# Kernel tuning notes

Hardware: AMD Instinct MI355X
Metric: run time of the kernel (lower is better)

Reference implementation:

```python
import jax, jax.numpy as jnp
from jax import lax
import numpy as np

S, B, I, H, O = 65536, 1, 2, 128, 1


def setup_inputs() -> dict:
    key = jax.random.key(0)
    k1, k2, k3, k4 = jax.random.split(key, 4)
    # xavier_normal-style scales
    s_ih = (2.0 / (4 * H + I)) ** 0.5
    s_hh = (2.0 / (4 * H + H)) ** 0.5
    s_out = (2.0 / (H + O)) ** 0.5
    return {
        "x": jax.random.normal(k1, (S, B, I), jnp.float32),
        "h0": jnp.zeros((1, B, H), jnp.float32),
        "c0": jnp.zeros((1, B, H), jnp.float32),
        "W_ih": jax.random.normal(k2, (4 * H, I), jnp.float32) * s_ih,
        "W_hh": jax.random.normal(k3, (4 * H, H), jnp.float32) * s_hh,
        "b_ih": jnp.zeros((4 * H,), jnp.float32),
        "b_hh": jnp.zeros((4 * H,), jnp.float32),
        "W_out": jax.random.normal(k4, (O, H), jnp.float32) * s_out,
        "b_out": jnp.zeros((O,), jnp.float32),
    }


def reference(x, h0, c0, W_ih, W_hh, b_ih, b_hh, W_out, b_out):
    # Precompute input-to-gate projections for all timesteps: (S, B, 4H)
    xg = jnp.einsum("sbi,gi->sbg", x, W_ih) + b_ih + b_hh

    def step(carry, xg_t):
        h, c = carry  # (B, H) each
        gates = xg_t + h @ W_hh.T  # (B, 4H); PyTorch order i,f,g,o
        i, f, g, o = jnp.split(gates, 4, axis=-1)
        i = jax.nn.sigmoid(i)
        f = jax.nn.sigmoid(f)
        g = jnp.tanh(g)
        o = jax.nn.sigmoid(o)
        c = f * c + i * g
        h = o * jnp.tanh(c)
        return (h, c), h

    (_, _), hs = lax.scan(step, (h0[0], c0[0]), xg)  # hs: (S, B, H)
    out = jnp.tanh(hs.transpose(1, 0, 2))  # (B, S, H), matches permute(1,0,2)
    out = out @ W_out.T + b_out  # (B, S, O)
    return out.reshape(out.shape[0] * out.shape[1], -1)  # (B*S, O)
```

## Files before the change

kernel.cpp:

```cpp
#include <hip/hip_runtime.h>

#define S_LEN 65536
#define HDIM 128

typedef _Float16 half2_t __attribute__((ext_vector_type(2)));
typedef _Float16 half8_t __attribute__((ext_vector_type(8)));
typedef float f32x4 __attribute__((ext_vector_type(4)));

__device__ __forceinline__ float sigm(float x) {
    return 1.0f / (1.0f + __expf(-x));
}
__device__ __forceinline__ float tanh_fast(float x) {
    return 2.0f / (1.0f + __expf(-2.0f * x)) - 1.0f;
}
__device__ __forceinline__ float dot2(half2_t a, half2_t b, float c) {
#if __has_builtin(__builtin_amdgcn_fdot2)
    return __builtin_amdgcn_fdot2(a, b, c, false);
#else
    return fmaf((float)a.x, (float)b.x, fmaf((float)a.y, (float)b.y, c));
#endif
}

#define WG_BARRIER() do {                                         \
    asm volatile("s_waitcnt lgkmcnt(0)" ::: "memory");            \
    __builtin_amdgcn_s_barrier();                                 \
    asm volatile("" ::: "memory");                                \
} while (0)

__global__ __launch_bounds__(256)
__attribute__((amdgpu_waves_per_eu(1, 1)))
void lstm_seq_dot(const float* __restrict__ x,
                  const float* __restrict__ h0,
                  const float* __restrict__ c0,
                  const float* __restrict__ W_ih,
                  const float* __restrict__ W_hh,
                  const float* __restrict__ b_ih,
                  const float* __restrict__ b_hh,
                  _Float16* __restrict__ h_hist)
{
    __shared__ __align__(16) _Float16 h_buf[2][HDIM];

    const int tid  = threadIdx.x;
    const int lane = tid & 63;
    const int w    = tid >> 6;
    const int j    = lane & 31;
    const int half = lane >> 5;
    const int hidx = w * 32 + j;
    const int k0   = half * 64;

#define LOAD_WF(g, c) \
    half8_t wf_##g##_##c; { \
        const float* s_ = W_hh + (size_t)(hidx + 128 * (g)) * HDIM \
                               + k0 + 8 * (c); \
        wf_##g##_##c = (half8_t){ \
            (_Float16)s_[0], (_Float16)s_[1], (_Float16)s_[2], (_Float16)s_[3], \
            (_Float16)s_[4], (_Float16)s_[5], (_Float16)s_[6], (_Float16)s_[7] }; \
        asm volatile("" : "+v"(wf_##g##_##c)); }
    LOAD_WF(0,0) LOAD_WF(0,1) LOAD_WF(0,2) LOAD_WF(0,3)
    LOAD_WF(0,4) LOAD_WF(0,5) LOAD_WF(0,6) LOAD_WF(0,7)
    LOAD_WF(1,0) LOAD_WF(1,1) LOAD_WF(1,2) LOAD_WF(1,3)
    LOAD_WF(1,4) LOAD_WF(1,5) LOAD_WF(1,6) LOAD_WF(1,7)
    LOAD_WF(2,0) LOAD_WF(2,1) LOAD_WF(2,2) LOAD_WF(2,3)
    LOAD_WF(2,4) LOAD_WF(2,5) LOAD_WF(2,6) LOAD_WF(2,7)
    LOAD_WF(3,0) LOAD_WF(3,1) LOAD_WF(3,2) LOAD_WF(3,3)
    LOAD_WF(3,4) LOAD_WF(3,5) LOAD_WF(3,6) LOAD_WF(3,7)
#undef LOAD_WF

    const int r0 = hidx, r1 = hidx + 128, r2 = hidx + 256, r3 = hidx + 384;
    const float wi00 = W_ih[2 * r0], wi01 = W_ih[2 * r0 + 1];
    const float wi10 = W_ih[2 * r1], wi11 = W_ih[2 * r1 + 1];
    const float wi20 = W_ih[2 * r2], wi21 = W_ih[2 * r2 + 1];
    const float wi30 = W_ih[2 * r3], wi31 = W_ih[2 * r3 + 1];
    const float bs0 = b_ih[r0] + b_hh[r0];
    const float bs1 = b_ih[r1] + b_hh[r1];
    const float bs2 = b_ih[r2] + b_hh[r2];
    const float bs3 = b_ih[r3] + b_hh[r3];
    float c = c0[hidx];

    if (tid < HDIM) h_buf[0][tid] = (_Float16)h0[tid];
    __syncthreads();

    const float2* xp = (const float2*)x;
    float2 xcur = xp[0];
    float2 xn1  = xp[1];

    const half8_t* hb0 = ((const half8_t*)h_buf[0]) + 8 * half;
    const half8_t* hb1 = ((const half8_t*)h_buf[1]) + 8 * half;

    _Float16* hh = h_hist + hidx;

#define DOT8(acc, wv, hv) \
    acc = dot2((half2_t){wv[0], wv[1]}, (half2_t){hv[0], hv[1]}, acc); \
    acc = dot2((half2_t){wv[2], wv[3]}, (half2_t){hv[2], hv[3]}, acc); \
    acc = dot2((half2_t){wv[4], wv[5]}, (half2_t){hv[4], hv[5]}, acc); \
    acc = dot2((half2_t){wv[6], wv[7]}, (half2_t){hv[6], hv[7]}, acc);

#define DCHUNK(a0_, a1_, a2_, a3_, c_, hv) \
    DOT8(a0_, wf_0_##c_, hv) \
    DOT8(a1_, wf_1_##c_, hv) \
    DOT8(a2_, wf_2_##c_, hv) \
    DOT8(a3_, wf_3_##c_, hv)

#define STEP(T, RB, WB, OFF) { \
     \
    half8_t hv0 = (RB)[0], hv1 = (RB)[1], hv2 = (RB)[2], hv3 = (RB)[3]; \
    half8_t hv4 = (RB)[4], hv5 = (RB)[5], hv6 = (RB)[6], hv7 = (RB)[7]; \
    int tn_ = (T) + 2; if (tn_ >= S_LEN) tn_ = S_LEN - 1; \
    float2 xnew_ = xp[tn_]; \
     \
    const float xg0 = fmaf(wi00, xcur.x, fmaf(wi01, xcur.y, bs0)); \
    const float xg1 = fmaf(wi10, xcur.x, fmaf(wi11, xcur.y, bs1)); \
    const float xg2 = fmaf(wi20, xcur.x, fmaf(wi21, xcur.y, bs2)); \
    const float xg3 = fmaf(wi30, xcur.x, fmaf(wi31, xcur.y, bs3)); \
    float sA0 = 0.f, sA1 = 0.f, sA2 = 0.f, sA3 = 0.f; \
    float sB0 = 0.f, sB1 = 0.f, sB2 = 0.f, sB3 = 0.f; \
    DCHUNK(sA0, sA1, sA2, sA3, 0, hv0) \
    DCHUNK(sB0, sB1, sB2, sB3, 1, hv1) \
    DCHUNK(sA0, sA1, sA2, sA3, 2, hv2) \
    DCHUNK(sB0, sB1, sB2, sB3, 3, hv3) \
    DCHUNK(sA0, sA1, sA2, sA3, 4, hv4) \
    DCHUNK(sB0, sB1, sB2, sB3, 5, hv5) \
    DCHUNK(sA0, sA1, sA2, sA3, 6, hv6) \
    DCHUNK(sB0, sB1, sB2, sB3, 7, hv7) \
    float s0 = sA0 + sB0; \
    float s1 = sA1 + sB1; \
    float s2 = sA2 + sB2; \
    float s3 = sA3 + sB3; \
     \
    s0 += __shfl_xor(s0, 32, 64); \
    s1 += __shfl_xor(s1, 32, 64); \
    s2 += __shfl_xor(s2, 32, 64); \
    s3 += __shfl_xor(s3, 32, 64); \
    const float gi = sigm(s0 + xg0); \
    const float gf = sigm(s1 + xg1); \
    const float gg = tanh_fast(s2 + xg2); \
    const float go = sigm(s3 + xg3); \
    c = fmaf(gf, c, gi * gg); \
    const float hvx_ = go * tanh_fast(c); \
    const _Float16 hf_ = (_Float16)hvx_; \
    if (lane < 32) { \
        (WB)[hidx] = hf_;                  \
        hh[OFF] = hf_;                     \
    } \
    xcur = xn1; xn1 = xnew_; \
    WG_BARRIER(); }

    #pragma unroll 1
    for (int t = 0; t < S_LEN; t += 2) {
        STEP(t,     hb0, h_buf[1], 0)
        STEP(t + 1, hb1, h_buf[0], HDIM)
        hh += 2 * HDIM;
    }
#undef STEP
#undef DCHUNK
#undef DOT8
}

__global__ __launch_bounds__(256)
void out_proj(const _Float16* __restrict__ h_hist,
              const float* __restrict__ W_out,
              const float* __restrict__ b_out,
              float* __restrict__ out)
{
    const int lane  = threadIdx.x & 63;
    const int gwave = (blockIdx.x * 256 + threadIdx.x) >> 6;
    const int nwave = (gridDim.x * 256) >> 6;

    const float wo0 = W_out[2 * lane + 0];
    const float wo1 = W_out[2 * lane + 1];
    const float bout = b_out[0];

    for (int t = gwave; t < S_LEN; t += nwave) {
        half2_t hv = ((const half2_t*)(h_hist + t * HDIM))[lane];
        float p = tanh_fast((float)hv.x) * wo0 + tanh_fast((float)hv.y) * wo1;
        #pragma unroll
        for (int off = 32; off > 0; off >>= 1)
            p += __shfl_xor(p, off, 64);
        if (lane == 0) out[t] = p + bout;
    }
}

#define H_HI_OFF 144
__global__ __launch_bounds__(1024)
__attribute__((amdgpu_waves_per_eu(4, 4)))
void lstm_seq_full(const float* __restrict__ x,
                   const float* __restrict__ h0,
                   const float* __restrict__ c0,
                   const float* __restrict__ W_ih,
                   const float* __restrict__ W_hh,
                   const float* __restrict__ b_ih,
                   const float* __restrict__ b_hh,
                   const float* __restrict__ W_out,
                   const float* __restrict__ b_out,
                   float* __restrict__ out)
{
    __shared__ __align__(16) unsigned char h_raw[2 * H_HI_OFF];
    __shared__ float gates_part[2 * 512];
    __shared__ float red_sh[2];

    const int tid  = threadIdx.x;
    const int j    = tid >> 1;
    const int half = tid & 1;

    const float2* wr2 = (const float2*)(W_hh + j * HDIM + half * 64);
#define WDEF(i) half2_t W##i; { float2 t = wr2[i]; \
        W##i.x = (_Float16)t.x; W##i.y = (_Float16)t.y; } \
        asm volatile("" : "+v"(W##i));
    WDEF(0)  WDEF(1)  WDEF(2)  WDEF(3)  WDEF(4)  WDEF(5)  WDEF(6)  WDEF(7)
    WDEF(8)  WDEF(9)  WDEF(10) WDEF(11) WDEF(12) WDEF(13) WDEF(14) WDEF(15)
    WDEF(16) WDEF(17) WDEF(18) WDEF(19) WDEF(20) WDEF(21) WDEF(22) WDEF(23)
    WDEF(24) WDEF(25) WDEF(26) WDEF(27) WDEF(28) WDEF(29) WDEF(30) WDEF(31)
#undef WDEF

    float wih0 = 0.0f, wih1 = 0.0f, bias = 0.0f;
    if (half == 0) {
        wih0 = W_ih[2 * j + 0];
        wih1 = W_ih[2 * j + 1];
        bias = b_ih[j] + b_hh[j];
    }

    float c = 0.0f, wout = 0.0f;
    _Float16* hw = (_Float16*)(h_raw + ((tid < 64) ? 2 * tid
                                                   : H_HI_OFF + 2 * (tid - 64)));
    if (tid < HDIM) {
        c = c0[tid];
        wout = W_out[tid];
        *hw = (_Float16)h0[tid];
    }
    const float bout = b_out[0];
    __syncthreads();

    const float2* xp = (const float2*)x;
    float2 xcur = xp[0];
    const half8_t* hp = (const half8_t*)(h_raw + half * H_HI_OFF);

    #pragma unroll 1
    for (int t = 0; t < S_LEN; ++t) {
        const int tn = (t + 1 < S_LEN) ? (t + 1) : (S_LEN - 1);
        float2 xnext = xp[tn];

        float a0 = fmaf(wih0, xcur.x, fmaf(wih1, xcur.y, bias));
        float a1 = 0.0f, a2 = 0.0f, a3 = 0.0f;

#define CHUNK(cc, w0_, w1_, w2_, w3_) {                         \
        half8_t hv = hp[cc];                                    \
        half2_t p0 = { hv[0], hv[1] };                          \
        half2_t p1 = { hv[2], hv[3] };                          \
        half2_t p2 = { hv[4], hv[5] };                          \
        half2_t p3 = { hv[6], hv[7] };                          \
        a0 = dot2(w0_, p0, a0);                                 \
        a1 = dot2(w1_, p1, a1);                                 \
        a2 = dot2(w2_, p2, a2);                                 \
        a3 = dot2(w3_, p3, a3); }
        CHUNK(0, W0,  W1,  W2,  W3)
        CHUNK(1, W4,  W5,  W6,  W7)
        CHUNK(2, W8,  W9,  W10, W11)
        CHUNK(3, W12, W13, W14, W15)
        CHUNK(4, W16, W17, W18, W19)
        CHUNK(5, W20, W21, W22, W23)
        CHUNK(6, W24, W25, W26, W27)
        CHUNK(7, W28, W29, W30, W31)
#undef CHUNK

        gates_part[half * 512 + j] = (a0 + a1) + (a2 + a3);
        __syncthreads();

        if (tid < HDIM) {
            float gi = sigm(gates_part[tid]            + gates_part[tid + 512]);
            float gf = sigm(gates_part[tid + 128]      + gates_part[tid + 640]);
            float gg = tanh_fast(gates_part[tid + 256] + gates_part[tid + 768]);
            float go = sigm(gates_part[tid + 384]      + gates_part[tid + 896]);
            c = fmaf(gf, c, gi * gg);
            float h = go * tanh_fast(c);
            *hw = (_Float16)h;

            float p = tanh_fast(h) * wout;
            #pragma unroll
            for (int off = 32; off > 0; off >>= 1)
                p += __shfl_xor(p, off, 64);
            if ((tid & 63) == 0) red_sh[tid >> 6] = p;
        }
        __syncthreads();

        if (tid == 0) out[t] = red_sh[0] + red_sh[1] + bout;
        xcur = xnext;
    }
}

extern "C" void kernel_launch(void* const* d_in, const int* in_sizes, int n_in,
                              void* d_out, int out_size, void* d_ws, size_t ws_size,
                              hipStream_t stream) {
    const float* x     = (const float*)d_in[0];
    const float* h0    = (const float*)d_in[1];
    const float* c0    = (const float*)d_in[2];
    const float* W_ih  = (const float*)d_in[3];
    const float* W_hh  = (const float*)d_in[4];
    const float* b_ih  = (const float*)d_in[5];
    const float* b_hh  = (const float*)d_in[6];
    const float* W_out = (const float*)d_in[7];
    const float* b_out = (const float*)d_in[8];

    const size_t need = (size_t)S_LEN * HDIM * sizeof(_Float16);
    if (ws_size >= need) {
        _Float16* h_hist = (_Float16*)d_ws;
        lstm_seq_dot<<<dim3(1), dim3(256), 0, stream>>>(
            x, h0, c0, W_ih, W_hh, b_ih, b_hh, h_hist);
        out_proj<<<dim3(1024), dim3(256), 0, stream>>>(
            h_hist, W_out, b_out, (float*)d_out);
    } else {
        lstm_seq_full<<<dim3(1), dim3(1024), 0, stream>>>(
            x, h0, c0, W_ih, W_hh, b_ih, b_hh, W_out, b_out, (float*)d_out);
    }
}
```

Before: 41.27 ms.

## Offload x staging and h history stores to a dedicated helper wave

Adds a fifth wave to the single-block LSTM kernel. It stages x into a double-buffered LDS ring and copies each new h from LDS to global h_hist in lockstep with the compute waves' barriers. This takes global loads and stores off the recurrent critical path of the four compute waves. The dot products are also restructured: weights are held as half2 registers and summed with four independent accumulators per gate, and the shuffle reduction is interleaved per gate. The trade-off is an extra wave taking part in every barrier, plus the LDS staging logic.

New measurement: 42.00 ms. No clear change (+1.8%).

```diff
diff --git a/kernel.cpp b/kernel.cpp
--- a/kernel.cpp
+++ b/kernel.cpp
@@ -27,133 +27,147 @@
     asm volatile("" ::: "memory");                                \
 } while (0)
 
-__global__ __launch_bounds__(256)
-__attribute__((amdgpu_waves_per_eu(1, 1)))
-void lstm_seq_dot(const float* __restrict__ x,
-                  const float* __restrict__ h0,
-                  const float* __restrict__ c0,
-                  const float* __restrict__ W_ih,
-                  const float* __restrict__ W_hh,
-                  const float* __restrict__ b_ih,
-                  const float* __restrict__ b_hh,
-                  _Float16* __restrict__ h_hist)
+__global__ __launch_bounds__(320)
+__attribute__((amdgpu_waves_per_eu(2)))
+void lstm_seq_dot2(const float* __restrict__ x,
+                   const float* __restrict__ h0,
+                   const float* __restrict__ c0,
+                   const float* __restrict__ W_ih,
+                   const float* __restrict__ W_hh,
+                   const float* __restrict__ b_ih,
+                   const float* __restrict__ b_hh,
+                   _Float16* __restrict__ h_hist)
 {
     __shared__ __align__(16) _Float16 h_buf[2][HDIM];
+    __shared__ __align__(16) float xb[1024];
 
     const int tid  = threadIdx.x;
     const int lane = tid & 63;
     const int w    = tid >> 6;
-    const int j    = lane & 31;
-    const int half = lane >> 5;
-    const int hidx = w * 32 + j;
-    const int k0   = half * 64;
-
-#define LOAD_WF(g, c) \
-    half8_t wf_##g##_##c; { \
-        const float* s_ = W_hh + (size_t)(hidx + 128 * (g)) * HDIM \
-                               + k0 + 8 * (c); \
-        wf_##g##_##c = (half8_t){ \
-            (_Float16)s_[0], (_Float16)s_[1], (_Float16)s_[2], (_Float16)s_[3], \
-            (_Float16)s_[4], (_Float16)s_[5], (_Float16)s_[6], (_Float16)s_[7] }; \
-        asm volatile("" : "+v"(wf_##g##_##c)); }
-    LOAD_WF(0,0) LOAD_WF(0,1) LOAD_WF(0,2) LOAD_WF(0,3)
-    LOAD_WF(0,4) LOAD_WF(0,5) LOAD_WF(0,6) LOAD_WF(0,7)
-    LOAD_WF(1,0) LOAD_WF(1,1) LOAD_WF(1,2) LOAD_WF(1,3)
-    LOAD_WF(1,4) LOAD_WF(1,5) LOAD_WF(1,6) LOAD_WF(1,7)
-    LOAD_WF(2,0) LOAD_WF(2,1) LOAD_WF(2,2) LOAD_WF(2,3)
-    LOAD_WF(2,4) LOAD_WF(2,5) LOAD_WF(2,6) LOAD_WF(2,7)
-    LOAD_WF(3,0) LOAD_WF(3,1) LOAD_WF(3,2) LOAD_WF(3,3)
-    LOAD_WF(3,4) LOAD_WF(3,5) LOAD_WF(3,6) LOAD_WF(3,7)
-#undef LOAD_WF
-
-    const int r0 = hidx, r1 = hidx + 128, r2 = hidx + 256, r3 = hidx + 384;
-    const float wi00 = W_ih[2 * r0], wi01 = W_ih[2 * r0 + 1];
-    const float wi10 = W_ih[2 * r1], wi11 = W_ih[2 * r1 + 1];
-    const float wi20 = W_ih[2 * r2], wi21 = W_ih[2 * r2 + 1];
-    const float wi30 = W_ih[2 * r3], wi31 = W_ih[2 * r3 + 1];
-    const float bs0 = b_ih[r0] + b_hh[r0];
-    const float bs1 = b_ih[r1] + b_hh[r1];
-    const float bs2 = b_ih[r2] + b_hh[r2];
-    const float bs3 = b_ih[r3] + b_hh[r3];
-    float c = c0[hidx];
-
-    if (tid < HDIM) h_buf[0][tid] = (_Float16)h0[tid];
-    __syncthreads();
-
-    const float2* xp = (const float2*)x;
-    float2 xcur = xp[0];
-    float2 xn1  = xp[1];
-
-    const half8_t* hb0 = ((const half8_t*)h_buf[0]) + 8 * half;
-    const half8_t* hb1 = ((const half8_t*)h_buf[1]) + 8 * half;
-
-    _Float16* hh = h_hist + hidx;
-
-#define DOT8(acc, wv, hv) \
-    acc = dot2((half2_t){wv[0], wv[1]}, (half2_t){hv[0], hv[1]}, acc); \
-    acc = dot2((half2_t){wv[2], wv[3]}, (half2_t){hv[2], hv[3]}, acc); \
-    acc = dot2((half2_t){wv[4], wv[5]}, (half2_t){hv[4], hv[5]}, acc); \
-    acc = dot2((half2_t){wv[6], wv[7]}, (half2_t){hv[6], hv[7]}, acc);
-
-#define DCHUNK(a0_, a1_, a2_, a3_, c_, hv) \
-    DOT8(a0_, wf_0_##c_, hv) \
-    DOT8(a1_, wf_1_##c_, hv) \
-    DOT8(a2_, wf_2_##c_, hv) \
-    DOT8(a3_, wf_3_##c_, hv)
-
-#define STEP(T, RB, WB, OFF) { \
-     \
-    half8_t hv0 = (RB)[0], hv1 = (RB)[1], hv2 = (RB)[2], hv3 = (RB)[3]; \
-    half8_t hv4 = (RB)[4], hv5 = (RB)[5], hv6 = (RB)[6], hv7 = (RB)[7]; \
-    int tn_ = (T) + 2; if (tn_ >= S_LEN) tn_ = S_LEN - 1; \
-    float2 xnew_ = xp[tn_]; \
-     \
-    const float xg0 = fmaf(wi00, xcur.x, fmaf(wi01, xcur.y, bs0)); \
-    const float xg1 = fmaf(wi10, xcur.x, fmaf(wi11, xcur.y, bs1)); \
-    const float xg2 = fmaf(wi20, xcur.x, fmaf(wi21, xcur.y, bs2)); \
-    const float xg3 = fmaf(wi30, xcur.x, fmaf(wi31, xcur.y, bs3)); \
-    float sA0 = 0.f, sA1 = 0.f, sA2 = 0.f, sA3 = 0.f; \
-    float sB0 = 0.f, sB1 = 0.f, sB2 = 0.f, sB3 = 0.f; \
-    DCHUNK(sA0, sA1, sA2, sA3, 0, hv0) \
-    DCHUNK(sB0, sB1, sB2, sB3, 1, hv1) \
-    DCHUNK(sA0, sA1, sA2, sA3, 2, hv2) \
-    DCHUNK(sB0, sB1, sB2, sB3, 3, hv3) \
-    DCHUNK(sA0, sA1, sA2, sA3, 4, hv4) \
-    DCHUNK(sB0, sB1, sB2, sB3, 5, hv5) \
-    DCHUNK(sA0, sA1, sA2, sA3, 6, hv6) \
-    DCHUNK(sB0, sB1, sB2, sB3, 7, hv7) \
-    float s0 = sA0 + sB0; \
-    float s1 = sA1 + sB1; \
-    float s2 = sA2 + sB2; \
-    float s3 = sA3 + sB3; \
-     \
-    s0 += __shfl_xor(s0, 32, 64); \
-    s1 += __shfl_xor(s1, 32, 64); \
-    s2 += __shfl_xor(s2, 32, 64); \
-    s3 += __shfl_xor(s3, 32, 64); \
-    const float gi = sigm(s0 + xg0); \
-    const float gf = sigm(s1 + xg1); \
-    const float gg = tanh_fast(s2 + xg2); \
-    const float go = sigm(s3 + xg3); \
-    c = fmaf(gf, c, gi * gg); \
-    const float hvx_ = go * tanh_fast(c); \
-    const _Float16 hf_ = (_Float16)hvx_; \
-    if (lane < 32) { \
-        (WB)[hidx] = hf_;                  \
-        hh[OFF] = hf_;                     \
-    } \
-    xcur = xn1; xn1 = xnew_; \
-    WG_BARRIER(); }
-
-    #pragma unroll 1
-    for (int t = 0; t < S_LEN; t += 2) {
-        STEP(t,     hb0, h_buf[1], 0)
-        STEP(t + 1, hb1, h_buf[0], HDIM)
-        hh += 2 * HDIM;
-    }
+
+    if (w < 4) {
+        const int j    = lane & 31;
+        const int half = lane >> 5;
+        const int hidx = w * 32 + j;
+        const int k0   = half * 64;
+
+#define LW2(g, k2) \
+        half2_t w_##g##_##k2; { \
+            const float* s_ = W_hh + (size_t)(hidx + 128 * (g)) * HDIM \
+                                   + k0 + 2 * (k2); \
+            w_##g##_##k2 = (half2_t){ (_Float16)s_[0], (_Float16)s_[1] }; \
+            asm volatile("" : "+v"(w_##g##_##k2)); }
+#define LWG(g) \
+        LW2(g,0)  LW2(g,1)  LW2(g,2)  LW2(g,3)  LW2(g,4)  LW2(g,5)  LW2(g,6)  LW2(g,7)  \
+        LW2(g,8)  LW2(g,9)  LW2(g,10) LW2(g,11) LW2(g,12) LW2(g,13) LW2(g,14) LW2(g,15) \
+        LW2(g,16) LW2(g,17) LW2(g,18) LW2(g,19) LW2(g,20) LW2(g,21) LW2(g,22) LW2(g,23) \
+        LW2(g,24) LW2(g,25) LW2(g,26) LW2(g,27) LW2(g,28) LW2(g,29) LW2(g,30) LW2(g,31)
+        LWG(0) LWG(1) LWG(2) LWG(3)
+#undef LWG
+#undef LW2
+
+        const int r0 = hidx, r1 = hidx + 128, r2 = hidx + 256, r3 = hidx + 384;
+        const float wi00 = W_ih[2 * r0], wi01 = W_ih[2 * r0 + 1];
+        const float wi10 = W_ih[2 * r1], wi11 = W_ih[2 * r1 + 1];
+        const float wi20 = W_ih[2 * r2], wi21 = W_ih[2 * r2 + 1];
+        const float wi30 = W_ih[2 * r3], wi31 = W_ih[2 * r3 + 1];
+        const float bs0 = b_ih[r0] + b_hh[r0];
+        const float bs1 = b_ih[r1] + b_hh[r1];
+        const float bs2 = b_ih[r2] + b_hh[r2];
+        const float bs3 = b_ih[r3] + b_hh[r3];
+        float c = c0[hidx];
+
+        if (tid < HDIM) h_buf[0][tid] = (_Float16)h0[tid];
+        __syncthreads();
+
+        const half8_t* hb0 = ((const half8_t*)h_buf[0]) + 8 * half;
+        const half8_t* hb1 = ((const half8_t*)h_buf[1]) + 8 * half;
+
+#define PR(hv, p) ((half2_t)__builtin_shufflevector((hv), (hv), 2*(p), 2*(p)+1))
+
+#define GDOT(g, dst) { \
+        float A_=0.f, B_=0.f, C_=0.f, D_=0.f; \
+        A_=dot2(w_##g##_0 , PR(hv0,0), A_); B_=dot2(w_##g##_1 , PR(hv0,1), B_); \
+        C_=dot2(w_##g##_2 , PR(hv0,2), C_); D_=dot2(w_##g##_3 , PR(hv0,3), D_); \
+        A_=dot2(w_##g##_4 , PR(hv1,0), A_); B_=dot2(w_##g##_5 , PR(hv1,1), B_); \
+        C_=dot2(w_##g##_6 , PR(hv1,2), C_); D_=dot2(w_##g##_7 , PR(hv1,3), D_); \
+        A_=dot2(w_##g##_8 , PR(hv2,0), A_); B_=dot2(w_##g##_9 , PR(hv2,1), B_); \
+        C_=dot2(w_##g##_10, PR(hv2,2), C_); D_=dot2(w_##g##_11, PR(hv2,3), D_); \
+        A_=dot2(w_##g##_12, PR(hv3,0), A_); B_=dot2(w_##g##_13, PR(hv3,1), B_); \
+        C_=dot2(w_##g##_14, PR(hv3,2), C_); D_=dot2(w_##g##_15, PR(hv3,3), D_); \
+        A_=dot2(w_##g##_16, PR(hv4,0), A_); B_=dot2(w_##g##_17, PR(hv4,1), B_); \
+        C_=dot2(w_##g##_18, PR(hv4,2), C_); D_=dot2(w_##g##_19, PR(hv4,3), D_); \
+        A_=dot2(w_##g##_20, PR(hv5,0), A_); B_=dot2(w_##g##_21, PR(hv5,1), B_); \
+        C_=dot2(w_##g##_22, PR(hv5,2), C_); D_=dot2(w_##g##_23, PR(hv5,3), D_); \
+        A_=dot2(w_##g##_24, PR(hv6,0), A_); B_=dot2(w_##g##_25, PR(hv6,1), B_); \
+        C_=dot2(w_##g##_26, PR(hv6,2), C_); D_=dot2(w_##g##_27, PR(hv6,3), D_); \
+        A_=dot2(w_##g##_28, PR(hv7,0), A_); B_=dot2(w_##g##_29, PR(hv7,1), B_); \
+        C_=dot2(w_##g##_30, PR(hv7,2), C_); D_=dot2(w_##g##_31, PR(hv7,3), D_); \
+        dst = (A_ + B_) + (C_ + D_); }
+
+#define STEP(T, RB, WB) { \
+        const half8_t* hb_ = (RB); \
+        half8_t hv0 = hb_[0], hv1 = hb_[1], hv2 = hb_[2], hv3 = hb_[3]; \
+        half8_t hv4 = hb_[4], hv5 = hb_[5], hv6 = hb_[6], hv7 = hb_[7]; \
+        const float2 xv = *(const float2*)(xb + 2 * ((T) & 511)); \
+        float s0, s1, s2, s3; \
+        GDOT(1, s1)  s1 += __shfl_xor(s1, 32, 64); \
+        GDOT(0, s0)  s0 += __shfl_xor(s0, 32, 64); \
+        GDOT(2, s2)  s2 += __shfl_xor(s2, 32, 64); \
+        GDOT(3, s3)  s3 += __shfl_xor(s3, 32, 64); \
+        const float gf = sigm(fmaf(wi10, xv.x, fmaf(wi11, xv.y, bs1)) + s1); \
+        const float gi = sigm(fmaf(wi00, xv.x, fmaf(wi01, xv.y, bs0)) + s0); \
+        const float gg = tanh_fast(fmaf(wi20, xv.x, fmaf(wi21, xv.y, bs2)) + s2); \
+        const float go = sigm(fmaf(wi30, xv.x, fmaf(wi31, xv.y, bs3)) + s3); \
+        c = fmaf(gf, c, gi * gg); \
+        const float hval = go * tanh_fast(c); \
+        const _Float16 hf_ = (_Float16)hval; \
+        if (lane < 32) (WB)[hidx] = hf_; \
+        WG_BARRIER(); }
+
+        #pragma unroll 1
+        for (int t = 0; t < S_LEN; t += 2) {
+            STEP(t,     hb0, h_buf[1])
+            STEP(t + 1, hb1, h_buf[0])
+        }
 #undef STEP
-#undef DCHUNK
-#undef DOT8
+#undef GDOT
+#undef PR
+    } else {
+        {
+            const float4* src = (const float4*)x + lane;
+            float4 a0 = src[0], a1 = src[64], a2 = src[128], a3 = src[192];
+            float4* dst = (float4*)xb + lane;
+            dst[0] = a0; dst[64] = a1; dst[128] = a2; dst[192] = a3;
+        }
+        __syncthreads();
+
+        float4 xs0 = {0.f, 0.f, 0.f, 0.f}, xs1 = xs0;
+
+        #pragma unroll 1
+        for (int t = 0; t < S_LEN; ++t) {
+            const int r   = t & 255;
+            const int blk = t >> 8;
+            if (r == 0 && blk >= 1 && blk < 255) {
+                const float4* src = (const float4*)x
+                                  + (size_t)(blk + 1) * 128 + lane;
+                xs0 = src[0]; xs1 = src[64];
+            }
+            if (r == 128 && blk >= 1 && blk < 255) {
+                float4* dst = (float4*)xb + (((blk + 1) & 1) * 128) + lane;
+                dst[0] = xs0; dst[64] = xs1;
+            }
+            if (t > 0) {
+                const uint32_t hv_ =
+                    *(const uint32_t*)((const char*)(h_buf[t & 1]) + 4 * lane);
+                ((uint32_t*)h_hist)[(size_t)(t - 1) * 64 + lane] = hv_;
+            }
+            WG_BARRIER();
+        }
+        const uint32_t hv_ =
+            *(const uint32_t*)((const char*)(h_buf[0]) + 4 * lane);
+        ((uint32_t*)h_hist)[(size_t)(S_LEN - 1) * 64 + lane] = hv_;
+    }
 }
 
 __global__ __launch_bounds__(256)
@@ -303,7 +317,7 @@
     const size_t need = (size_t)S_LEN * HDIM * sizeof(_Float16);
     if (ws_size >= need) {
         _Float16* h_hist = (_Float16*)d_ws;
-        lstm_seq_dot<<<dim3(1), dim3(256), 0, stream>>>(
+        lstm_seq_dot2<<<dim3(1), dim3(320), 0, stream>>>(
             x, h0, c0, W_ih, W_hh, b_ih, b_hh, h_hist);
         out_proj<<<dim3(1024), dim3(256), 0, stream>>>(
             h_hist, W_out, b_out, (float*)d_out);
```
